# Optimization experiments

Hardware: AMD Instinct MI355X
Metric: run time of the kernel (lower is better)

The kernel has to match this reference:

```python
import jax, jax.numpy as jnp
import numpy as np

N_NODES = 100000
N_EDGES = 3200000
IN_CH = 256
OUT_CH = 10


def setup_inputs() -> dict:
    key = jax.random.key(0)
    k1, k2, k3, k4 = jax.random.split(key, 4)
    x = jax.random.normal(k1, (N_NODES, IN_CH), dtype=jnp.float32)
    edge_index = jax.random.randint(k2, (2, N_EDGES), 0, N_NODES, dtype=jnp.int64)
    W_mu = jax.random.normal(k3, (IN_CH, OUT_CH), dtype=jnp.float32) * (1.0 / np.sqrt(IN_CH))
    b_mu = jnp.zeros((OUT_CH,), dtype=jnp.float32)
    W_logstd = jax.random.normal(k4, (IN_CH, OUT_CH), dtype=jnp.float32) * (1.0 / np.sqrt(IN_CH))
    b_logstd = jnp.zeros((OUT_CH,), dtype=jnp.float32)
    return {"x": x, "edge_index": edge_index, "W_mu": W_mu, "b_mu": b_mu,
            "W_logstd": W_logstd, "b_logstd": b_logstd}


def _gcn_norm(edge_index, num_nodes):
    # PyG gcn_norm: add self loops, deg from target (col), norm = d^-1/2[row]*d^-1/2[col]
    loop = jnp.arange(num_nodes, dtype=edge_index.dtype)
    row = jnp.concatenate([edge_index[0], loop])  # source nodes
    col = jnp.concatenate([edge_index[1], loop])  # target nodes
    deg = jax.ops.segment_sum(jnp.ones_like(col, dtype=jnp.float32), col,
                              num_segments=num_nodes)
    dinv = jax.lax.rsqrt(jnp.maximum(deg, 1.0))  # self loops guarantee deg>=1
    norm = dinv[row] * dinv[col]  # [E+N]
    return row, col, norm


def _gcn_conv(x, W, b, row, col, norm, num_nodes):
    h = x @ W                               # [N, out]  linear transform first
    msg = h[row] * norm[:, None]            # gather + scale, [E+N, out]
    out = jax.ops.segment_sum(msg, col, num_segments=num_nodes)  # scatter-add
    return out + b


def reference(x, edge_index, W_mu, b_mu, W_logstd, b_logstd):
    n = x.shape[0]
    row, col, norm = _gcn_norm(edge_index, n)
    mu = _gcn_conv(x, W_mu, b_mu, row, col, norm, n)
    logstd = _gcn_conv(x, W_logstd, b_logstd, row, col, norm, n)
    return mu, logstd
```

## Files before the change

### kernel.cpp

```cpp
#include <hip/hip_runtime.h>
#include <math.h>

#define N_NODES 100000
#define N_EDGES 3200000
#define IN_CH 256
#define NC 20
#define OC 10
#define NPB 128
#define NBUCK 782
#define CAP 4864

#define CHUNK3 8192
#define NCHUNK3 391

__global__ __launch_bounds__(256) void k_initptr(int* __restrict__ bptr) {
    int i = blockIdx.x * 256 + threadIdx.x;
    if (i < NBUCK) bptr[i] = i * CAP;
}

__global__ __launch_bounds__(1024) void k_bin3(const int* __restrict__ row,
                                               const int* __restrict__ col,
                                               int* __restrict__ bptr,
                                               int* __restrict__ bpairs) {
    __shared__ int   lh[NBUCK];
    __shared__ int   lscan[NBUCK];
    __shared__ int   gmino[NBUCK];
    __shared__ int   stage[CHUNK3];
    __shared__ unsigned short sbkt[CHUNK3];

    int t = threadIdx.x;
    int e0 = blockIdx.x * CHUNK3;
    int nE = N_EDGES - e0; if (nE > CHUNK3) nE = CHUNK3;
    int n4 = nE >> 2;
    const int4* c4 = (const int4*)(col + e0);
    const int4* r4 = (const int4*)(row + e0);

    for (int i = t; i < NBUCK; i += 1024) lh[i] = 0;
    __syncthreads();

    for (int j = t; j < n4; j += 1024) {
        int4 c = c4[j];
        atomicAdd(&lh[c.x >> 7], 1); atomicAdd(&lh[c.y >> 7], 1);
        atomicAdd(&lh[c.z >> 7], 1); atomicAdd(&lh[c.w >> 7], 1);
    }
    __syncthreads();

    int cnt = 0;
    if (t < NBUCK) { cnt = lh[t]; lscan[t] = cnt; }
    __syncthreads();
    for (int o = 1; o < NBUCK; o <<= 1) {
        int add = 0;
        if (t < NBUCK && t >= o) add = lscan[t - o];
        __syncthreads();
        if (t < NBUCK) lscan[t] += add;
        __syncthreads();
    }
    if (t < NBUCK) {
        int lofs = lscan[t] - cnt;
        int gbase = cnt ? atomicAdd(&bptr[t], cnt) : 0;
        gmino[t] = gbase - lofs;
        lh[t] = lofs;
    }
    __syncthreads();

    for (int j = t; j < n4; j += 1024) {
        int4 c = c4[j];
        int4 r = r4[j];
        int b0 = c.x >> 7, b1 = c.y >> 7, b2 = c.z >> 7, b3 = c.w >> 7;
        int s0 = atomicAdd(&lh[b0], 1);
        int s1 = atomicAdd(&lh[b1], 1);
        int s2 = atomicAdd(&lh[b2], 1);
        int s3 = atomicAdd(&lh[b3], 1);
        stage[s0] = (r.x << 7) | (c.x & 127); sbkt[s0] = (unsigned short)b0;
        stage[s1] = (r.y << 7) | (c.y & 127); sbkt[s1] = (unsigned short)b1;
        stage[s2] = (r.z << 7) | (c.z & 127); sbkt[s2] = (unsigned short)b2;
        stage[s3] = (r.w << 7) | (c.w & 127); sbkt[s3] = (unsigned short)b3;
    }
    __syncthreads();

    for (int j = t; j < nE; j += 1024) {
        int b = sbkt[j];
        int dst = gmino[b] + j;
        if (dst < (b + 1) * CAP) bpairs[dst] = stage[j];
    }
}

__global__ __launch_bounds__(256) void k_deg(const int* __restrict__ bptr,
                                             const int* __restrict__ bpairs,
                                             float* __restrict__ dinv) {
    __shared__ int lc[NPB];
    int b = blockIdx.x, t = threadIdx.x;
    if (t < NPB) lc[t] = 0;
    __syncthreads();
    int start = b * CAP;
    int n = bptr[b] - start; if (n > CAP) n = CAP;
    for (int p = t; p < n; p += 256)
        atomicAdd(&lc[bpairs[start + p] & 127], 1);
    __syncthreads();
    int node = b * NPB + t;
    if (t < NPB && node < N_NODES)
        dinv[node] = rsqrtf((float)(lc[t] + 1));
}

__device__ __forceinline__ unsigned bfpack(float a, float b) {
    unsigned ua = __float_as_uint(a), ub = __float_as_uint(b);
    ua = (ua + 0x7FFFu + ((ua >> 16) & 1u)) >> 16;
    ub = (ub + 0x7FFFu + ((ub >> 16) & 1u)) >> 16;
    return ua | (ub << 16);
}
__device__ __forceinline__ float bflo(unsigned p) { return __uint_as_float(p << 16); }
__device__ __forceinline__ float bfhi(unsigned p) { return __uint_as_float(p & 0xFFFF0000u); }

__global__ __launch_bounds__(256) void k_gemm6s(const float* __restrict__ x,
                                                const float* __restrict__ Wmu,
                                                const float* __restrict__ Wls,
                                                const float* __restrict__ dinv,
                                                uint4* __restrict__ hbA,
                                                uint4* __restrict__ hbB,
                                                uint2* __restrict__ hbC) {
    __shared__ float sW[NC * 272];
    int t = threadIdx.x;
    for (int idx = t; idx < IN_CH * OC; idx += 256) {
        int k = idx / OC, c = idx - (idx / OC) * OC;
        int kk = k >> 6, j = k & 63;
        sW[c * 272 + kk * 68 + j]          = Wmu[idx];
        sW[(c + OC) * 272 + kk * 68 + j]   = Wls[idx];
    }
    __syncthreads();

    int kk = t & 3;
    int slot = t >> 2;
    int n0 = blockIdx.x * 128 + slot;

    int nd[2];
#pragma unroll
    for (int u = 0; u < 2; u++) {
        int n = n0 + u * 64;
        nd[u] = (n < N_NODES) ? n : (N_NODES - 1);
    }

    float acc[2][NC];
#pragma unroll
    for (int u = 0; u < 2; u++)
#pragma unroll
        for (int c = 0; c < NC; c++) acc[u][c] = 0.0f;

    const float4* x4 = (const float4*)x;

#pragma unroll 4
    for (int j4 = 0; j4 < 16; j4++) {
        float4 xv0 = x4[(size_t)nd[0] * 64 + kk * 16 + j4];
        float4 xv1 = x4[(size_t)nd[1] * 64 + kk * 16 + j4];
#pragma unroll
        for (int c = 0; c < NC; c++) {
            float4 w = *(const float4*)&sW[c * 272 + kk * 68 + j4 * 4];
            acc[0][c] += xv0.x * w.x + xv0.y * w.y + xv0.z * w.z + xv0.w * w.w;
            acc[1][c] += xv1.x * w.x + xv1.y * w.y + xv1.z * w.z + xv1.w * w.w;
        }
    }

#pragma unroll
    for (int u = 0; u < 2; u++)
#pragma unroll
        for (int c = 0; c < NC; c++) {
            acc[u][c] += __shfl_xor(acc[u][c], 2);
            acc[u][c] += __shfl_xor(acc[u][c], 1);
        }

    if (kk == 0) {
#pragma unroll
        for (int u = 0; u < 2; u++) {
            int n = n0 + u * 64;
            if (n >= N_NODES) continue;
            float d = dinv[n];
            hbA[n] = make_uint4(bfpack(acc[u][0] * d,  acc[u][1] * d),
                                bfpack(acc[u][2] * d,  acc[u][3] * d),
                                bfpack(acc[u][4] * d,  acc[u][5] * d),
                                bfpack(acc[u][6] * d,  acc[u][7] * d));
            hbB[n] = make_uint4(bfpack(acc[u][8] * d,  acc[u][9] * d),
                                bfpack(acc[u][10] * d, acc[u][11] * d),
                                bfpack(acc[u][12] * d, acc[u][13] * d),
                                bfpack(acc[u][14] * d, acc[u][15] * d));
            hbC[n] = make_uint2(bfpack(acc[u][16] * d, acc[u][17] * d),
                                bfpack(acc[u][18] * d, acc[u][19] * d));
        }
    }
}

__global__ __launch_bounds__(512) void k_agg7(const int* __restrict__ bptr,
                                              const int* __restrict__ bpairs,
                                              const uint4* __restrict__ hbA,
                                              const uint4* __restrict__ hbB,
                                              const uint2* __restrict__ hbC,
                                              const float* __restrict__ bmu,
                                              const float* __restrict__ bls,
                                              float* __restrict__ out) {
    __shared__ int lcnt[NPB];
    __shared__ int lscan[NPB];
    __shared__ int sCnt[NPB];
    __shared__ int ssrc[CAP];
    int b = blockIdx.x, t = threadIdx.x;
    int start = b * CAP;
    int n = bptr[b] - start; if (n > CAP) n = CAP;

    if (t < NPB) lcnt[t] = 0;
    __syncthreads();
    for (int p = t; p < n; p += 512)
        atomicAdd(&lcnt[bpairs[start + p] & 127], 1);
    __syncthreads();

    int cnt = 0;
    if (t < NPB) { cnt = lcnt[t]; lscan[t] = cnt; sCnt[t] = cnt; }
    __syncthreads();
    for (int o = 1; o < NPB; o <<= 1) {
        int add = 0;
        if (t < NPB && t >= o) add = lscan[t - o];
        __syncthreads();
        if (t < NPB) lscan[t] += add;
        __syncthreads();
    }
    if (t < NPB) lcnt[t] = lscan[t] - cnt;
    __syncthreads();

    for (int p = t; p < n; p += 512) {
        int pk = bpairs[start + p];
        int q = atomicAdd(&lcnt[pk & 127], 1);
        ssrc[q] = ((unsigned)pk) >> 7;
    }
    __syncthreads();

    int nl = t >> 2, quarter = t & 3;
    int node = b * NPB + nl;
    int ccnt = sCnt[nl];
    int base = lscan[nl] - ccnt;
    int j0 = (ccnt * quarter) >> 2;
    int j1 = (ccnt * (quarter + 1)) >> 2;

    float a[NC];
#pragma unroll
    for (int c = 0; c < NC; c++) a[c] = 0.0f;

#define ADDROW(R)                                                        \
    {                                                                    \
        uint4 qa = hbA[(R)];                                             \
        uint4 qb = hbB[(R)];                                             \
        uint2 qc = hbC[(R)];                                             \
        a[0]  += bflo(qa.x); a[1]  += bfhi(qa.x);                        \
        a[2]  += bflo(qa.y); a[3]  += bfhi(qa.y);                        \
        a[4]  += bflo(qa.z); a[5]  += bfhi(qa.z);                        \
        a[6]  += bflo(qa.w); a[7]  += bfhi(qa.w);                        \
        a[8]  += bflo(qb.x); a[9]  += bfhi(qb.x);                        \
        a[10] += bflo(qb.y); a[11] += bfhi(qb.y);                        \
        a[12] += bflo(qb.z); a[13] += bfhi(qb.z);                        \
        a[14] += bflo(qb.w); a[15] += bfhi(qb.w);                        \
        a[16] += bflo(qc.x); a[17] += bfhi(qc.x);                        \
        a[18] += bflo(qc.y); a[19] += bfhi(qc.y);                        \
    }

    int j = j0;
    for (; j + 1 < j1; j += 2) {
        int r0 = ssrc[base + j];
        int r1 = ssrc[base + j + 1];
        ADDROW(r0);
        ADDROW(r1);
    }
    if (j < j1) {
        int r0 = ssrc[base + j];
        ADDROW(r0);
    }
    if (quarter == 0 && node < N_NODES) ADDROW(node);
#undef ADDROW

#pragma unroll
    for (int c = 0; c < NC; c++) {
        a[c] += __shfl_xor(a[c], 1);
        a[c] += __shfl_xor(a[c], 2);
    }

    if (quarter == 0 && node < N_NODES) {
        float dn = rsqrtf((float)(ccnt + 1));
        float* om = out + (size_t)node * OC;
        float* ol = out + (size_t)N_NODES * OC + (size_t)node * OC;
#pragma unroll
        for (int c = 0; c < OC; c++) {
            om[c] = dn * a[c]      + bmu[c];
            ol[c] = dn * a[c + OC] + bls[c];
        }
    }
}

__global__ __launch_bounds__(256) void k_init_deg(float* __restrict__ deg) {
    int i = blockIdx.x * 256 + threadIdx.x;
    if (i < N_NODES) deg[i] = 1.0f;
}
__global__ __launch_bounds__(256) void k_count(const int* __restrict__ col, float* __restrict__ deg) {
    int e = blockIdx.x * 256 + threadIdx.x;
    if (e < N_EDGES) atomicAdd(&deg[col[e]], 1.0f);
}
__global__ __launch_bounds__(256) void k_dinvk(float* __restrict__ deg) {
    int i = blockIdx.x * 256 + threadIdx.x;
    if (i < N_NODES) deg[i] = rsqrtf(deg[i]);
}
__global__ __launch_bounds__(256) void k_gemm_f32(const float* __restrict__ x,
                                                  const float* __restrict__ Wmu,
                                                  const float* __restrict__ Wls,
                                                  float* __restrict__ h) {
    int node = blockIdx.x * 256 + threadIdx.x;
    if (node >= N_NODES) return;
    const float4* x4 = (const float4*)(x + (size_t)node * IN_CH);
    float acc[NC];
#pragma unroll
    for (int c = 0; c < NC; c++) acc[c] = 0.0f;
    for (int k4 = 0; k4 < IN_CH / 4; k4++) {
        float4 xv = x4[k4];
        float xk[4] = {xv.x, xv.y, xv.z, xv.w};
#pragma unroll
        for (int kk = 0; kk < 4; kk++) {
            const float* wm = Wmu + (k4 * 4 + kk) * OC;
            const float* wl = Wls + (k4 * 4 + kk) * OC;
#pragma unroll
            for (int c = 0; c < OC; c++) {
                acc[c]      += xk[kk] * wm[c];
                acc[c + OC] += xk[kk] * wl[c];
            }
        }
    }
    float* hp = h + (size_t)node * NC;
#pragma unroll
    for (int c = 0; c < NC; c++) hp[c] = acc[c];
}
__global__ __launch_bounds__(256) void k_scatter(const int* __restrict__ row, const int* __restrict__ col,
                                                 const float* __restrict__ dinv, const float* __restrict__ h,
                                                 float* __restrict__ out) {
    int e = blockIdx.x * 256 + threadIdx.x;
    if (e >= N_EDGES) return;
    int r = row[e], c = col[e];
    float s = dinv[r] * dinv[c];
    const float* hp = h + (size_t)r * NC;
    float* om = out + (size_t)c * OC;
    float* ol = om + (size_t)N_NODES * OC;
#pragma unroll
    for (int k = 0; k < OC; k++) atomicAdd(om + k, hp[k] * s);
#pragma unroll
    for (int k = 0; k < OC; k++) atomicAdd(ol + k, hp[OC + k] * s);
}
__global__ __launch_bounds__(256) void k_final(const float* __restrict__ h, const float* __restrict__ dinv,
                                               const float* __restrict__ bmu, const float* __restrict__ bls,
                                               float* __restrict__ out) {
    int i = blockIdx.x * 256 + threadIdx.x;
    if (i >= N_NODES * OC) return;
    int node = i / OC, c = i - node * OC;
    float d = dinv[node];
    float d2 = d * d;
    out[i]                += h[node * NC + c]      * d2 + bmu[c];
    out[N_NODES * OC + i] += h[node * NC + OC + c] * d2 + bls[c];
}

extern "C" void kernel_launch(void* const* d_in, const int* in_sizes, int n_in,
                              void* d_out, int out_size, void* d_ws, size_t ws_size,
                              hipStream_t stream) {
    const float* x   = (const float*)d_in[0];
    const int*   ei  = (const int*)d_in[1];
    const float* Wmu = (const float*)d_in[2];
    const float* bmu = (const float*)d_in[3];
    const float* Wls = (const float*)d_in[4];
    const float* bls = (const float*)d_in[5];
    float* out = (float*)d_out;

    const int* row = ei;
    const int* col = ei + N_EDGES;

    const size_t BPAIRS_OFF = (size_t)(9 << 19);
    const size_t REQ = BPAIRS_OFF + (size_t)NBUCK * CAP * 4;

    if (ws_size >= REQ) {
        char* w = (char*)d_ws;
        int*      bptr   = (int*)(w);
        float*    dinv   = (float*)(w + 8192);
        uint4*    hbA    = (uint4*)(w + (512 << 10));
        uint4*    hbB    = (uint4*)(w + (512 << 10) + 1600000);
        uint2*    hbC    = (uint2*)(w + (512 << 10) + 3200000);
        int*      bpairs = (int*)(w + BPAIRS_OFF);

        k_initptr<<<(NBUCK + 255) / 256, 256, 0, stream>>>(bptr);
        k_bin3<<<NCHUNK3, 1024, 0, stream>>>(row, col, bptr, bpairs);
        k_deg<<<NBUCK, 256, 0, stream>>>(bptr, bpairs, dinv);
        k_gemm6s<<<(N_NODES + 127) / 128, 256, 0, stream>>>(x, Wmu, Wls, dinv, hbA, hbB, hbC);
        k_agg7<<<NBUCK, 512, 0, stream>>>(bptr, bpairs, hbA, hbB, hbC, bmu, bls, out);
    } else {
        float* deg = (float*)d_ws;
        float* h   = (float*)((char*)d_ws + (1 << 20));
        hipMemsetAsync(d_out, 0, (size_t)out_size * sizeof(float), stream);
        k_init_deg<<<(N_NODES + 255) / 256, 256, 0, stream>>>(deg);
        k_count<<<(N_EDGES + 255) / 256, 256, 0, stream>>>(col, deg);
        k_dinvk<<<(N_NODES + 255) / 256, 256, 0, stream>>>(deg);
        k_gemm_f32<<<(N_NODES + 255) / 256, 256, 0, stream>>>(x, Wmu, Wls, h);
        k_scatter<<<(N_EDGES + 255) / 256, 256, 0, stream>>>(row, col, deg, h, out);
        k_final<<<(N_NODES * OC + 255) / 256, 256, 0, stream>>>(h, deg, bmu, bls, out);
    }
}
```

Baseline: 283.4 us.

## Fuse edge binning and GEMM into one heterogeneous kernel, move dinv scaling to aggregation

```diff
diff --git a/kernel.cpp b/kernel.cpp
--- a/kernel.cpp
+++ b/kernel.cpp
@@ -12,76 +12,170 @@
 
 #define CHUNK3 8192
 #define NCHUNK3 391
+#define NGEMMB 196
+#define NMEGA 587
 
 __global__ __launch_bounds__(256) void k_initptr(int* __restrict__ bptr) {
     int i = blockIdx.x * 256 + threadIdx.x;
     if (i < NBUCK) bptr[i] = i * CAP;
 }
 
-__global__ __launch_bounds__(1024) void k_bin3(const int* __restrict__ row,
+__device__ __forceinline__ unsigned bfpack(float a, float b) {
+    unsigned ua = __float_as_uint(a), ub = __float_as_uint(b);
+    ua = (ua + 0x7FFFu + ((ua >> 16) & 1u)) >> 16;
+    ub = (ub + 0x7FFFu + ((ub >> 16) & 1u)) >> 16;
+    return ua | (ub << 16);
+}
+__device__ __forceinline__ float bflo(unsigned p) { return __uint_as_float(p << 16); }
+__device__ __forceinline__ float bfhi(unsigned p) { return __uint_as_float(p & 0xFFFF0000u); }
+
+struct BinSmem {
+    int lh[NBUCK];
+    int lscan[NBUCK];
+    int gmino[NBUCK];
+    int stage[CHUNK3];
+    unsigned short sbkt[CHUNK3];
+};
+struct GemmSmem { float sW[NC * 272]; };
+union MegaSmem { BinSmem b; GemmSmem g; };
+
+__global__ __launch_bounds__(1024) void k_mega(const int* __restrict__ row,
                                                const int* __restrict__ col,
                                                int* __restrict__ bptr,
-                                               int* __restrict__ bpairs) {
-    __shared__ int   lh[NBUCK];
-    __shared__ int   lscan[NBUCK];
-    __shared__ int   gmino[NBUCK];
-    __shared__ int   stage[CHUNK3];
-    __shared__ unsigned short sbkt[CHUNK3];
-
+                                               int* __restrict__ bpairs,
+                                               const float* __restrict__ x,
+                                               const float* __restrict__ Wmu,
+                                               const float* __restrict__ Wls,
+                                               uint4* __restrict__ hbA,
+                                               uint4* __restrict__ hbB,
+                                               uint2* __restrict__ hbC) {
+    __shared__ MegaSmem sm;
+    int bid = blockIdx.x;
     int t = threadIdx.x;
-    int e0 = blockIdx.x * CHUNK3;
-    int nE = N_EDGES - e0; if (nE > CHUNK3) nE = CHUNK3;
-    int n4 = nE >> 2;
-    const int4* c4 = (const int4*)(col + e0);
-    const int4* r4 = (const int4*)(row + e0);
-
-    for (int i = t; i < NBUCK; i += 1024) lh[i] = 0;
-    __syncthreads();
-
-    for (int j = t; j < n4; j += 1024) {
-        int4 c = c4[j];
-        atomicAdd(&lh[c.x >> 7], 1); atomicAdd(&lh[c.y >> 7], 1);
-        atomicAdd(&lh[c.z >> 7], 1); atomicAdd(&lh[c.w >> 7], 1);
-    }
-    __syncthreads();
-
-    int cnt = 0;
-    if (t < NBUCK) { cnt = lh[t]; lscan[t] = cnt; }
-    __syncthreads();
-    for (int o = 1; o < NBUCK; o <<= 1) {
-        int add = 0;
-        if (t < NBUCK && t >= o) add = lscan[t - o];
-        __syncthreads();
-        if (t < NBUCK) lscan[t] += add;
-        __syncthreads();
-    }
-    if (t < NBUCK) {
-        int lofs = lscan[t] - cnt;
-        int gbase = cnt ? atomicAdd(&bptr[t], cnt) : 0;
-        gmino[t] = gbase - lofs;
-        lh[t] = lofs;
-    }
-    __syncthreads();
-
-    for (int j = t; j < n4; j += 1024) {
-        int4 c = c4[j];
-        int4 r = r4[j];
-        int b0 = c.x >> 7, b1 = c.y >> 7, b2 = c.z >> 7, b3 = c.w >> 7;
-        int s0 = atomicAdd(&lh[b0], 1);
-        int s1 = atomicAdd(&lh[b1], 1);
-        int s2 = atomicAdd(&lh[b2], 1);
-        int s3 = atomicAdd(&lh[b3], 1);
-        stage[s0] = (r.x << 7) | (c.x & 127); sbkt[s0] = (unsigned short)b0;
-        stage[s1] = (r.y << 7) | (c.y & 127); sbkt[s1] = (unsigned short)b1;
-        stage[s2] = (r.z << 7) | (c.z & 127); sbkt[s2] = (unsigned short)b2;
-        stage[s3] = (r.w << 7) | (c.w & 127); sbkt[s3] = (unsigned short)b3;
-    }
-    __syncthreads();
-
-    for (int j = t; j < nE; j += 1024) {
-        int b = sbkt[j];
-        int dst = gmino[b] + j;
-        if (dst < (b + 1) * CAP) bpairs[dst] = stage[j];
+    bool isGemm = (bid < 2 * NGEMMB) && (bid & 1);
+
+    if (!isGemm) {
+        int cb = (bid < 2 * NGEMMB) ? (bid >> 1) : (bid - NGEMMB);
+        int e0 = cb * CHUNK3;
+        int nE = N_EDGES - e0; if (nE > CHUNK3) nE = CHUNK3;
+        int n4 = nE >> 2;
+        const int4* c4 = (const int4*)(col + e0);
+        const int4* r4 = (const int4*)(row + e0);
+
+        for (int i = t; i < NBUCK; i += 1024) sm.b.lh[i] = 0;
+        __syncthreads();
+
+        for (int j = t; j < n4; j += 1024) {
+            int4 c = c4[j];
+            atomicAdd(&sm.b.lh[c.x >> 7], 1); atomicAdd(&sm.b.lh[c.y >> 7], 1);
+            atomicAdd(&sm.b.lh[c.z >> 7], 1); atomicAdd(&sm.b.lh[c.w >> 7], 1);
+        }
+        __syncthreads();
+
+        int cnt = 0;
+        if (t < NBUCK) { cnt = sm.b.lh[t]; sm.b.lscan[t] = cnt; }
+        __syncthreads();
+        for (int o = 1; o < NBUCK; o <<= 1) {
+            int add = 0;
+            if (t < NBUCK && t >= o) add = sm.b.lscan[t - o];
+            __syncthreads();
+            if (t < NBUCK) sm.b.lscan[t] += add;
+            __syncthreads();
+        }
+        if (t < NBUCK) {
+            int lofs = sm.b.lscan[t] - cnt;
+            int gbase = cnt ? atomicAdd(&bptr[t], cnt) : 0;
+            sm.b.gmino[t] = gbase - lofs;
+            sm.b.lh[t] = lofs;
+        }
+        __syncthreads();
+
+        for (int j = t; j < n4; j += 1024) {
+            int4 c = c4[j];
+            int4 r = r4[j];
+            int b0 = c.x >> 7, b1 = c.y >> 7, b2 = c.z >> 7, b3 = c.w >> 7;
+            int s0 = atomicAdd(&sm.b.lh[b0], 1);
+            int s1 = atomicAdd(&sm.b.lh[b1], 1);
+            int s2 = atomicAdd(&sm.b.lh[b2], 1);
+            int s3 = atomicAdd(&sm.b.lh[b3], 1);
+            sm.b.stage[s0] = (r.x << 7) | (c.x & 127); sm.b.sbkt[s0] = (unsigned short)b0;
+            sm.b.stage[s1] = (r.y << 7) | (c.y & 127); sm.b.sbkt[s1] = (unsigned short)b1;
+            sm.b.stage[s2] = (r.z << 7) | (c.z & 127); sm.b.sbkt[s2] = (unsigned short)b2;
+            sm.b.stage[s3] = (r.w << 7) | (c.w & 127); sm.b.sbkt[s3] = (unsigned short)b3;
+        }
+        __syncthreads();
+
+        for (int j = t; j < nE; j += 1024) {
+            int b = sm.b.sbkt[j];
+            int dst = sm.b.gmino[b] + j;
+            if (dst < (b + 1) * CAP) bpairs[dst] = sm.b.stage[j];
+        }
+    } else {
+        int gb = bid >> 1;
+        for (int idx = t; idx < IN_CH * OC; idx += 1024) {
+            int k = idx / OC, c = idx - (idx / OC) * OC;
+            int kk = k >> 6, j = k & 63;
+            sm.g.sW[c * 272 + kk * 68 + j]        = Wmu[idx];
+            sm.g.sW[(c + OC) * 272 + kk * 68 + j] = Wls[idx];
+        }
+        __syncthreads();
+
+        int kk = t & 3;
+        int slot = t >> 2;
+        int n0 = gb * 512 + slot;
+
+        int nd[2];
+#pragma unroll
+        for (int u = 0; u < 2; u++) {
+            int n = n0 + u * 256;
+            nd[u] = (n < N_NODES) ? n : (N_NODES - 1);
+        }
+
+        float acc[2][NC];
+#pragma unroll
+        for (int u = 0; u < 2; u++)
+#pragma unroll
+            for (int c = 0; c < NC; c++) acc[u][c] = 0.0f;
+
+        const float4* x4 = (const float4*)x;
+
+#pragma unroll 4
+        for (int j4 = 0; j4 < 16; j4++) {
+            float4 xv0 = x4[(size_t)nd[0] * 64 + kk * 16 + j4];
+            float4 xv1 = x4[(size_t)nd[1] * 64 + kk * 16 + j4];
+#pragma unroll
+            for (int c = 0; c < NC; c++) {
+                float4 w = *(const float4*)&sm.g.sW[c * 272 + kk * 68 + j4 * 4];
+                acc[0][c] += xv0.x * w.x + xv0.y * w.y + xv0.z * w.z + xv0.w * w.w;
+                acc[1][c] += xv1.x * w.x + xv1.y * w.y + xv1.z * w.z + xv1.w * w.w;
+            }
+        }
+
+#pragma unroll
+        for (int u = 0; u < 2; u++)
+#pragma unroll
+            for (int c = 0; c < NC; c++) {
+                acc[u][c] += __shfl_xor(acc[u][c], 2);
+                acc[u][c] += __shfl_xor(acc[u][c], 1);
+            }
+
+        if (kk == 0) {
+#pragma unroll
+            for (int u = 0; u < 2; u++) {
+                int n = n0 + u * 256;
+                if (n >= N_NODES) continue;
+                hbA[n] = make_uint4(bfpack(acc[u][0],  acc[u][1]),
+                                    bfpack(acc[u][2],  acc[u][3]),
+                                    bfpack(acc[u][4],  acc[u][5]),
+                                    bfpack(acc[u][6],  acc[u][7]));
+                hbB[n] = make_uint4(bfpack(acc[u][8],  acc[u][9]),
+                                    bfpack(acc[u][10], acc[u][11]),
+                                    bfpack(acc[u][12], acc[u][13]),
+                                    bfpack(acc[u][14], acc[u][15]));
+                hbC[n] = make_uint2(bfpack(acc[u][16], acc[u][17]),
+                                    bfpack(acc[u][18], acc[u][19]));
+            }
+        }
     }
 }
 
@@ -102,96 +196,12 @@
         dinv[node] = rsqrtf((float)(lc[t] + 1));
 }
 
-__device__ __forceinline__ unsigned bfpack(float a, float b) {
-    unsigned ua = __float_as_uint(a), ub = __float_as_uint(b);
-    ua = (ua + 0x7FFFu + ((ua >> 16) & 1u)) >> 16;
-    ub = (ub + 0x7FFFu + ((ub >> 16) & 1u)) >> 16;
-    return ua | (ub << 16);
-}
-__device__ __forceinline__ float bflo(unsigned p) { return __uint_as_float(p << 16); }
-__device__ __forceinline__ float bfhi(unsigned p) { return __uint_as_float(p & 0xFFFF0000u); }
-
-__global__ __launch_bounds__(256) void k_gemm6s(const float* __restrict__ x,
-                                                const float* __restrict__ Wmu,
-                                                const float* __restrict__ Wls,
-                                                const float* __restrict__ dinv,
-                                                uint4* __restrict__ hbA,
-                                                uint4* __restrict__ hbB,
-                                                uint2* __restrict__ hbC) {
-    __shared__ float sW[NC * 272];
-    int t = threadIdx.x;
-    for (int idx = t; idx < IN_CH * OC; idx += 256) {
-        int k = idx / OC, c = idx - (idx / OC) * OC;
-        int kk = k >> 6, j = k & 63;
-        sW[c * 272 + kk * 68 + j]          = Wmu[idx];
-        sW[(c + OC) * 272 + kk * 68 + j]   = Wls[idx];
-    }
-    __syncthreads();
-
-    int kk = t & 3;
-    int slot = t >> 2;
-    int n0 = blockIdx.x * 128 + slot;
-
-    int nd[2];
-#pragma unroll
-    for (int u = 0; u < 2; u++) {
-        int n = n0 + u * 64;
-        nd[u] = (n < N_NODES) ? n : (N_NODES - 1);
-    }
-
-    float acc[2][NC];
-#pragma unroll
-    for (int u = 0; u < 2; u++)
-#pragma unroll
-        for (int c = 0; c < NC; c++) acc[u][c] = 0.0f;
-
-    const float4* x4 = (const float4*)x;
-
-#pragma unroll 4
-    for (int j4 = 0; j4 < 16; j4++) {
-        float4 xv0 = x4[(size_t)nd[0] * 64 + kk * 16 + j4];
-        float4 xv1 = x4[(size_t)nd[1] * 64 + kk * 16 + j4];
-#pragma unroll
-        for (int c = 0; c < NC; c++) {
-            float4 w = *(const float4*)&sW[c * 272 + kk * 68 + j4 * 4];
-            acc[0][c] += xv0.x * w.x + xv0.y * w.y + xv0.z * w.z + xv0.w * w.w;
-            acc[1][c] += xv1.x * w.x + xv1.y * w.y + xv1.z * w.z + xv1.w * w.w;
-        }
-    }
-
-#pragma unroll
-    for (int u = 0; u < 2; u++)
-#pragma unroll
-        for (int c = 0; c < NC; c++) {
-            acc[u][c] += __shfl_xor(acc[u][c], 2);
-            acc[u][c] += __shfl_xor(acc[u][c], 1);
-        }
-
-    if (kk == 0) {
-#pragma unroll
-        for (int u = 0; u < 2; u++) {
-            int n = n0 + u * 64;
-            if (n >= N_NODES) continue;
-            float d = dinv[n];
-            hbA[n] = make_uint4(bfpack(acc[u][0] * d,  acc[u][1] * d),
-                                bfpack(acc[u][2] * d,  acc[u][3] * d),
-                                bfpack(acc[u][4] * d,  acc[u][5] * d),
-                                bfpack(acc[u][6] * d,  acc[u][7] * d));
-            hbB[n] = make_uint4(bfpack(acc[u][8] * d,  acc[u][9] * d),
-                                bfpack(acc[u][10] * d, acc[u][11] * d),
-                                bfpack(acc[u][12] * d, acc[u][13] * d),
-                                bfpack(acc[u][14] * d, acc[u][15] * d));
-            hbC[n] = make_uint2(bfpack(acc[u][16] * d, acc[u][17] * d),
-                                bfpack(acc[u][18] * d, acc[u][19] * d));
-        }
-    }
-}
-
-__global__ __launch_bounds__(512) void k_agg7(const int* __restrict__ bptr,
+__global__ __launch_bounds__(512) void k_agg8(const int* __restrict__ bptr,
                                               const int* __restrict__ bpairs,
                                               const uint4* __restrict__ hbA,
                                               const uint4* __restrict__ hbB,
                                               const uint2* __restrict__ hbC,
+                                              const float* __restrict__ dinv,
                                               const float* __restrict__ bmu,
                                               const float* __restrict__ bls,
                                               float* __restrict__ out) {
@@ -240,35 +250,38 @@
 #pragma unroll
     for (int c = 0; c < NC; c++) a[c] = 0.0f;
 
-#define ADDROW(R)                                                        \
+#define ADDROW(R, S)                                                     \
     {                                                                    \
         uint4 qa = hbA[(R)];                                             \
         uint4 qb = hbB[(R)];                                             \
         uint2 qc = hbC[(R)];                                             \
-        a[0]  += bflo(qa.x); a[1]  += bfhi(qa.x);                        \
-        a[2]  += bflo(qa.y); a[3]  += bfhi(qa.y);                        \
-        a[4]  += bflo(qa.z); a[5]  += bfhi(qa.z);                        \
-        a[6]  += bflo(qa.w); a[7]  += bfhi(qa.w);                        \
-        a[8]  += bflo(qb.x); a[9]  += bfhi(qb.x);                        \
-        a[10] += bflo(qb.y); a[11] += bfhi(qb.y);                        \
-        a[12] += bflo(qb.z); a[13] += bfhi(qb.z);                        \
-        a[14] += bflo(qb.w); a[15] += bfhi(qb.w);                        \
-        a[16] += bflo(qc.x); a[17] += bfhi(qc.x);                        \
-        a[18] += bflo(qc.y); a[19] += bfhi(qc.y);                        \
+        float s_ = (S);                                                  \
+        a[0]  += s_ * bflo(qa.x); a[1]  += s_ * bfhi(qa.x);              \
+        a[2]  += s_ * bflo(qa.y); a[3]  += s_ * bfhi(qa.y);              \
+        a[4]  += s_ * bflo(qa.z); a[5]  += s_ * bfhi(qa.z);              \
+        a[6]  += s_ * bflo(qa.w); a[7]  += s_ * bfhi(qa.w);              \
+        a[8]  += s_ * bflo(qb.x); a[9]  += s_ * bfhi(qb.x);              \
+        a[10] += s_ * bflo(qb.y); a[11] += s_ * bfhi(qb.y);              \
+        a[12] += s_ * bflo(qb.z); a[13] += s_ * bfhi(qb.z);              \
+        a[14] += s_ * bflo(qb.w); a[15] += s_ * bfhi(qb.w);              \
+        a[16] += s_ * bflo(qc.x); a[17] += s_ * bfhi(qc.x);              \
+        a[18] += s_ * bflo(qc.y); a[19] += s_ * bfhi(qc.y);              \
     }
 
     int j = j0;
     for (; j + 1 < j1; j += 2) {
         int r0 = ssrc[base + j];
         int r1 = ssrc[base + j + 1];
-        ADDROW(r0);
-        ADDROW(r1);
+        float s0 = dinv[r0];
+        float s1 = dinv[r1];
+        ADDROW(r0, s0);
+        ADDROW(r1, s1);
     }
     if (j < j1) {
         int r0 = ssrc[base + j];
-        ADDROW(r0);
-    }
-    if (quarter == 0 && node < N_NODES) ADDROW(node);
+        ADDROW(r0, dinv[r0]);
+    }
+    if (quarter == 0 && node < N_NODES) ADDROW(node, dinv[node]);
 #undef ADDROW
 
 #pragma unroll
@@ -383,10 +396,9 @@
         int*      bpairs = (int*)(w + BPAIRS_OFF);
 
         k_initptr<<<(NBUCK + 255) / 256, 256, 0, stream>>>(bptr);
-        k_bin3<<<NCHUNK3, 1024, 0, stream>>>(row, col, bptr, bpairs);
+        k_mega<<<NMEGA, 1024, 0, stream>>>(row, col, bptr, bpairs, x, Wmu, Wls, hbA, hbB, hbC);
         k_deg<<<NBUCK, 256, 0, stream>>>(bptr, bpairs, dinv);
-        k_gemm6s<<<(N_NODES + 127) / 128, 256, 0, stream>>>(x, Wmu, Wls, dinv, hbA, hbB, hbC);
-        k_agg7<<<NBUCK, 512, 0, stream>>>(bptr, bpairs, hbA, hbB, hbC, bmu, bls, out);
+        k_agg8<<<NBUCK, 512, 0, stream>>>(bptr, bpairs, hbA, hbB, hbC, dinv, bmu, bls, out);
     } else {
         float* deg = (float*)d_ws;
         float* h   = (float*)((char*)d_ws + (1 << 20));
```

Result: slower. 309.9 us (+9.3%).

## Fuse edge binning and GEMM into one interleaved launch, defer dinv scaling

Applied to the files above, without the earlier changes.

```diff
diff --git a/kernel.cpp b/kernel.cpp
--- a/kernel.cpp
+++ b/kernel.cpp
@@ -12,94 +12,12 @@
 
 #define CHUNK3 8192
 #define NCHUNK3 391
+#define NGEMMB 196
+#define NMEGA 587
 
 __global__ __launch_bounds__(256) void k_initptr(int* __restrict__ bptr) {
     int i = blockIdx.x * 256 + threadIdx.x;
     if (i < NBUCK) bptr[i] = i * CAP;
-}
-
-__global__ __launch_bounds__(1024) void k_bin3(const int* __restrict__ row,
-                                               const int* __restrict__ col,
-                                               int* __restrict__ bptr,
-                                               int* __restrict__ bpairs) {
-    __shared__ int   lh[NBUCK];
-    __shared__ int   lscan[NBUCK];
-    __shared__ int   gmino[NBUCK];
-    __shared__ int   stage[CHUNK3];
-    __shared__ unsigned short sbkt[CHUNK3];
-
-    int t = threadIdx.x;
-    int e0 = blockIdx.x * CHUNK3;
-    int nE = N_EDGES - e0; if (nE > CHUNK3) nE = CHUNK3;
-    int n4 = nE >> 2;
-    const int4* c4 = (const int4*)(col + e0);
-    const int4* r4 = (const int4*)(row + e0);
-
-    for (int i = t; i < NBUCK; i += 1024) lh[i] = 0;
-    __syncthreads();
-
-    for (int j = t; j < n4; j += 1024) {
-        int4 c = c4[j];
-        atomicAdd(&lh[c.x >> 7], 1); atomicAdd(&lh[c.y >> 7], 1);
-        atomicAdd(&lh[c.z >> 7], 1); atomicAdd(&lh[c.w >> 7], 1);
-    }
-    __syncthreads();
-
-    int cnt = 0;
-    if (t < NBUCK) { cnt = lh[t]; lscan[t] = cnt; }
-    __syncthreads();
-    for (int o = 1; o < NBUCK; o <<= 1) {
-        int add = 0;
-        if (t < NBUCK && t >= o) add = lscan[t - o];
-        __syncthreads();
-        if (t < NBUCK) lscan[t] += add;
-        __syncthreads();
-    }
-    if (t < NBUCK) {
-        int lofs = lscan[t] - cnt;
-        int gbase = cnt ? atomicAdd(&bptr[t], cnt) : 0;
-        gmino[t] = gbase - lofs;
-        lh[t] = lofs;
-    }
-    __syncthreads();
-
-    for (int j = t; j < n4; j += 1024) {
-        int4 c = c4[j];
-        int4 r = r4[j];
-        int b0 = c.x >> 7, b1 = c.y >> 7, b2 = c.z >> 7, b3 = c.w >> 7;
-        int s0 = atomicAdd(&lh[b0], 1);
-        int s1 = atomicAdd(&lh[b1], 1);
-        int s2 = atomicAdd(&lh[b2], 1);
-        int s3 = atomicAdd(&lh[b3], 1);
-        stage[s0] = (r.x << 7) | (c.x & 127); sbkt[s0] = (unsigned short)b0;
-        stage[s1] = (r.y << 7) | (c.y & 127); sbkt[s1] = (unsigned short)b1;
-        stage[s2] = (r.z << 7) | (c.z & 127); sbkt[s2] = (unsigned short)b2;
-        stage[s3] = (r.w << 7) | (c.w & 127); sbkt[s3] = (unsigned short)b3;
-    }
-    __syncthreads();
-
-    for (int j = t; j < nE; j += 1024) {
-        int b = sbkt[j];
-        int dst = gmino[b] + j;
-        if (dst < (b + 1) * CAP) bpairs[dst] = stage[j];
-    }
-}
-
-__global__ __launch_bounds__(256) void k_deg(const int* __restrict__ bptr,
-                                             const int* __restrict__ bpairs,
-                                             float* __restrict__ dinv) {
-    __shared__ int lc[NPB];
-    int b = blockIdx.x, t = threadIdx.x;
-    if (t < NPB) lc[t] = 0;
-    __syncthreads();
-    int start = b * CAP;
-    int n = bptr[b] - start; if (n > CAP) n = CAP;
-    for (int p = t; p < n; p += 256)
-        atomicAdd(&lc[bpairs[start + p] & 127], 1);
-    __syncthreads();
-    int node = b * NPB + t;
-    if (t < NPB && node < N_NODES)
-        dinv[node] = rsqrtf((float)(lc[t] + 1));
 }
 
 __device__ __forceinline__ unsigned bfpack(float a, float b) {
@@ -111,79 +29,179 @@
 __device__ __forceinline__ float bflo(unsigned p) { return __uint_as_float(p << 16); }
 __device__ __forceinline__ float bfhi(unsigned p) { return __uint_as_float(p & 0xFFFF0000u); }
 
-__global__ __launch_bounds__(256) void k_gemm6s(const float* __restrict__ x,
-                                                const float* __restrict__ Wmu,
-                                                const float* __restrict__ Wls,
-                                                const float* __restrict__ dinv,
-                                                uint4* __restrict__ hbA,
-                                                uint4* __restrict__ hbB,
-                                                uint2* __restrict__ hbC) {
-    __shared__ float sW[NC * 272];
+struct BinSmem {
+    int lh[NBUCK];
+    int lscan[NBUCK];
+    int gmino[NBUCK];
+    int stage[CHUNK3];
+    unsigned short sbkt[CHUNK3];
+};
+struct GemmSmem { float sW[NC * 272]; };
+union MegaSmem { BinSmem b; GemmSmem g; };
+
+__global__ __launch_bounds__(1024) void k_mega32(const int* __restrict__ row,
+                                                 const int* __restrict__ col,
+                                                 int* __restrict__ bptr,
+                                                 int* __restrict__ bpairs,
+                                                 const float* __restrict__ x,
+                                                 const float* __restrict__ Wmu,
+                                                 const float* __restrict__ Wls,
+                                                 float* __restrict__ h32) {
+    __shared__ MegaSmem sm;
+    int bid = blockIdx.x;
     int t = threadIdx.x;
-    for (int idx = t; idx < IN_CH * OC; idx += 256) {
-        int k = idx / OC, c = idx - (idx / OC) * OC;
-        int kk = k >> 6, j = k & 63;
-        sW[c * 272 + kk * 68 + j]          = Wmu[idx];
-        sW[(c + OC) * 272 + kk * 68 + j]   = Wls[idx];
-    }
-    __syncthreads();
-
-    int kk = t & 3;
-    int slot = t >> 2;
-    int n0 = blockIdx.x * 128 + slot;
-
-    int nd[2];
-#pragma unroll
-    for (int u = 0; u < 2; u++) {
-        int n = n0 + u * 64;
-        nd[u] = (n < N_NODES) ? n : (N_NODES - 1);
-    }
-
-    float acc[2][NC];
-#pragma unroll
-    for (int u = 0; u < 2; u++)
-#pragma unroll
-        for (int c = 0; c < NC; c++) acc[u][c] = 0.0f;
-
-    const float4* x4 = (const float4*)x;
+    bool isGemm = (bid < 2 * NGEMMB) && (bid & 1);
+
+    if (!isGemm) {
+        int cb = (bid < 2 * NGEMMB) ? (bid >> 1) : (bid - NGEMMB);
+        int e0 = cb * CHUNK3;
+        int nE = N_EDGES - e0; if (nE > CHUNK3) nE = CHUNK3;
+        int n4 = nE >> 2;
+        const int4* c4 = (const int4*)(col + e0);
+        const int4* r4 = (const int4*)(row + e0);
+
+        for (int i = t; i < NBUCK; i += 1024) sm.b.lh[i] = 0;
+        __syncthreads();
+
+        for (int j = t; j < n4; j += 1024) {
+            int4 c = c4[j];
+            atomicAdd(&sm.b.lh[c.x >> 7], 1); atomicAdd(&sm.b.lh[c.y >> 7], 1);
+            atomicAdd(&sm.b.lh[c.z >> 7], 1); atomicAdd(&sm.b.lh[c.w >> 7], 1);
+        }
+        __syncthreads();
+
+        int cnt = 0;
+        if (t < NBUCK) { cnt = sm.b.lh[t]; sm.b.lscan[t] = cnt; }
+        __syncthreads();
+        for (int o = 1; o < NBUCK; o <<= 1) {
+            int add = 0;
+            if (t < NBUCK && t >= o) add = sm.b.lscan[t - o];
+            __syncthreads();
+            if (t < NBUCK) sm.b.lscan[t] += add;
+            __syncthreads();
+        }
+        if (t < NBUCK) {
+            int lofs = sm.b.lscan[t] - cnt;
+            int gbase = cnt ? atomicAdd(&bptr[t], cnt) : 0;
+            sm.b.gmino[t] = gbase - lofs;
+            sm.b.lh[t] = lofs;
+        }
+        __syncthreads();
+
+        for (int j = t; j < n4; j += 1024) {
+            int4 c = c4[j];
+            int4 r = r4[j];
+            int b0 = c.x >> 7, b1 = c.y >> 7, b2 = c.z >> 7, b3 = c.w >> 7;
+            int s0 = atomicAdd(&sm.b.lh[b0], 1);
+            int s1 = atomicAdd(&sm.b.lh[b1], 1);
+            int s2 = atomicAdd(&sm.b.lh[b2], 1);
+            int s3 = atomicAdd(&sm.b.lh[b3], 1);
+            sm.b.stage[s0] = (r.x << 7) | (c.x & 127); sm.b.sbkt[s0] = (unsigned short)b0;
+            sm.b.stage[s1] = (r.y << 7) | (c.y & 127); sm.b.sbkt[s1] = (unsigned short)b1;
+            sm.b.stage[s2] = (r.z << 7) | (c.z & 127); sm.b.sbkt[s2] = (unsigned short)b2;
+            sm.b.stage[s3] = (r.w << 7) | (c.w & 127); sm.b.sbkt[s3] = (unsigned short)b3;
+        }
+        __syncthreads();
+
+        for (int j = t; j < nE; j += 1024) {
+            int b = sm.b.sbkt[j];
+            int dst = sm.b.gmino[b] + j;
+            if (dst < (b + 1) * CAP) bpairs[dst] = sm.b.stage[j];
+        }
+    } else {
+        int gb = bid >> 1;
+        for (int idx = t; idx < IN_CH * OC; idx += 1024) {
+            int k = idx / OC, c = idx - (idx / OC) * OC;
+            int kk = k >> 6, j = k & 63;
+            sm.g.sW[c * 272 + kk * 68 + j]        = Wmu[idx];
+            sm.g.sW[(c + OC) * 272 + kk * 68 + j] = Wls[idx];
+        }
+        __syncthreads();
+
+        int kk = t & 3;
+        int slot = t >> 2;
+        int n0 = gb * 512 + slot;
+
+        int nd[2];
+#pragma unroll
+        for (int u = 0; u < 2; u++) {
+            int n = n0 + u * 256;
+            nd[u] = (n < N_NODES) ? n : (N_NODES - 1);
+        }
+
+        float acc[2][NC];
+#pragma unroll
+        for (int u = 0; u < 2; u++)
+#pragma unroll
+            for (int c = 0; c < NC; c++) acc[u][c] = 0.0f;
+
+        const float4* x4 = (const float4*)x;
 
 #pragma unroll 4
-    for (int j4 = 0; j4 < 16; j4++) {
-        float4 xv0 = x4[(size_t)nd[0] * 64 + kk * 16 + j4];
-        float4 xv1 = x4[(size_t)nd[1] * 64 + kk * 16 + j4];
-#pragma unroll
-        for (int c = 0; c < NC; c++) {
-            float4 w = *(const float4*)&sW[c * 272 + kk * 68 + j4 * 4];
-            acc[0][c] += xv0.x * w.x + xv0.y * w.y + xv0.z * w.z + xv0.w * w.w;
-            acc[1][c] += xv1.x * w.x + xv1.y * w.y + xv1.z * w.z + xv1.w * w.w;
-        }
-    }
-
-#pragma unroll
-    for (int u = 0; u < 2; u++)
-#pragma unroll
-        for (int c = 0; c < NC; c++) {
-            acc[u][c] += __shfl_xor(acc[u][c], 2);
-            acc[u][c] += __shfl_xor(acc[u][c], 1);
-        }
-
-    if (kk == 0) {
-#pragma unroll
-        for (int u = 0; u < 2; u++) {
-            int n = n0 + u * 64;
-            if (n >= N_NODES) continue;
-            float d = dinv[n];
-            hbA[n] = make_uint4(bfpack(acc[u][0] * d,  acc[u][1] * d),
-                                bfpack(acc[u][2] * d,  acc[u][3] * d),
-                                bfpack(acc[u][4] * d,  acc[u][5] * d),
-                                bfpack(acc[u][6] * d,  acc[u][7] * d));
-            hbB[n] = make_uint4(bfpack(acc[u][8] * d,  acc[u][9] * d),
-                                bfpack(acc[u][10] * d, acc[u][11] * d),
-                                bfpack(acc[u][12] * d, acc[u][13] * d),
-                                bfpack(acc[u][14] * d, acc[u][15] * d));
-            hbC[n] = make_uint2(bfpack(acc[u][16] * d, acc[u][17] * d),
-                                bfpack(acc[u][18] * d, acc[u][19] * d));
-        }
+        for (int j4 = 0; j4 < 16; j4++) {
+            float4 xv0 = x4[(size_t)nd[0] * 64 + kk * 16 + j4];
+            float4 xv1 = x4[(size_t)nd[1] * 64 + kk * 16 + j4];
+#pragma unroll
+            for (int c = 0; c < NC; c++) {
+                float4 w = *(const float4*)&sm.g.sW[c * 272 + kk * 68 + j4 * 4];
+                acc[0][c] += xv0.x * w.x + xv0.y * w.y + xv0.z * w.z + xv0.w * w.w;
+                acc[1][c] += xv1.x * w.x + xv1.y * w.y + xv1.z * w.z + xv1.w * w.w;
+            }
+        }
+
+#pragma unroll
+        for (int u = 0; u < 2; u++)
+#pragma unroll
+            for (int c = 0; c < NC; c++) {
+                acc[u][c] += __shfl_xor(acc[u][c], 2);
+                acc[u][c] += __shfl_xor(acc[u][c], 1);
+            }
+
+        if (kk == 0) {
+#pragma unroll
+            for (int u = 0; u < 2; u++) {
+                int n = n0 + u * 256;
+                if (n >= N_NODES) continue;
+                float* hp = h32 + (size_t)n * NC;
+                *(float4*)(hp + 0)  = make_float4(acc[u][0],  acc[u][1],  acc[u][2],  acc[u][3]);
+                *(float4*)(hp + 4)  = make_float4(acc[u][4],  acc[u][5],  acc[u][6],  acc[u][7]);
+                *(float4*)(hp + 8)  = make_float4(acc[u][8],  acc[u][9],  acc[u][10], acc[u][11]);
+                *(float4*)(hp + 12) = make_float4(acc[u][12], acc[u][13], acc[u][14], acc[u][15]);
+                *(float4*)(hp + 16) = make_float4(acc[u][16], acc[u][17], acc[u][18], acc[u][19]);
+            }
+        }
+    }
+}
+
+__global__ __launch_bounds__(256) void k_degs(const int* __restrict__ bptr,
+                                              const int* __restrict__ bpairs,
+                                              const float* __restrict__ h32,
+                                              uint4* __restrict__ hbA,
+                                              uint4* __restrict__ hbB,
+                                              uint2* __restrict__ hbC) {
+    __shared__ int lc[NPB];
+    int b = blockIdx.x, t = threadIdx.x;
+    if (t < NPB) lc[t] = 0;
+    __syncthreads();
+    int start = b * CAP;
+    int n = bptr[b] - start; if (n > CAP) n = CAP;
+    for (int p = t; p < n; p += 256)
+        atomicAdd(&lc[bpairs[start + p] & 127], 1);
+    __syncthreads();
+    int node = b * NPB + t;
+    if (t < NPB && node < N_NODES) {
+        float d = rsqrtf((float)(lc[t] + 1));
+        const float* hp = h32 + (size_t)node * NC;
+        float4 v0 = *(const float4*)(hp + 0);
+        float4 v1 = *(const float4*)(hp + 4);
+        float4 v2 = *(const float4*)(hp + 8);
+        float4 v3 = *(const float4*)(hp + 12);
+        float4 v4 = *(const float4*)(hp + 16);
+        hbA[node] = make_uint4(bfpack(v0.x * d, v0.y * d), bfpack(v0.z * d, v0.w * d),
+                               bfpack(v1.x * d, v1.y * d), bfpack(v1.z * d, v1.w * d));
+        hbB[node] = make_uint4(bfpack(v2.x * d, v2.y * d), bfpack(v2.z * d, v2.w * d),
+                               bfpack(v3.x * d, v3.y * d), bfpack(v3.z * d, v3.w * d));
+        hbC[node] = make_uint2(bfpack(v4.x * d, v4.y * d), bfpack(v4.z * d, v4.w * d));
     }
 }
 
@@ -289,6 +307,162 @@
     }
 }
 
+__global__ __launch_bounds__(1024) void k_bin3(const int* __restrict__ row,
+                                               const int* __restrict__ col,
+                                               int* __restrict__ bptr,
+                                               int* __restrict__ bpairs) {
+    __shared__ int   lh[NBUCK];
+    __shared__ int   lscan[NBUCK];
+    __shared__ int   gmino[NBUCK];
+    __shared__ int   stage[CHUNK3];
+    __shared__ unsigned short sbkt[CHUNK3];
+
+    int t = threadIdx.x;
+    int e0 = blockIdx.x * CHUNK3;
+    int nE = N_EDGES - e0; if (nE > CHUNK3) nE = CHUNK3;
+    int n4 = nE >> 2;
+    const int4* c4 = (const int4*)(col + e0);
+    const int4* r4 = (const int4*)(row + e0);
+
+    for (int i = t; i < NBUCK; i += 1024) lh[i] = 0;
+    __syncthreads();
+    for (int j = t; j < n4; j += 1024) {
+        int4 c = c4[j];
+        atomicAdd(&lh[c.x >> 7], 1); atomicAdd(&lh[c.y >> 7], 1);
+        atomicAdd(&lh[c.z >> 7], 1); atomicAdd(&lh[c.w >> 7], 1);
+    }
+    __syncthreads();
+    int cnt = 0;
+    if (t < NBUCK) { cnt = lh[t]; lscan[t] = cnt; }
+    __syncthreads();
+    for (int o = 1; o < NBUCK; o <<= 1) {
+        int add = 0;
+        if (t < NBUCK && t >= o) add = lscan[t - o];
+        __syncthreads();
+        if (t < NBUCK) lscan[t] += add;
+        __syncthreads();
+    }
+    if (t < NBUCK) {
+        int lofs = lscan[t] - cnt;
+        int gbase = cnt ? atomicAdd(&bptr[t], cnt) : 0;
+        gmino[t] = gbase - lofs;
+        lh[t] = lofs;
+    }
+    __syncthreads();
+    for (int j = t; j < n4; j += 1024) {
+        int4 c = c4[j];
+        int4 r = r4[j];
+        int b0 = c.x >> 7, b1 = c.y >> 7, b2 = c.z >> 7, b3 = c.w >> 7;
+        int s0 = atomicAdd(&lh[b0], 1);
+        int s1 = atomicAdd(&lh[b1], 1);
+        int s2 = atomicAdd(&lh[b2], 1);
+        int s3 = atomicAdd(&lh[b3], 1);
+        stage[s0] = (r.x << 7) | (c.x & 127); sbkt[s0] = (unsigned short)b0;
+        stage[s1] = (r.y << 7) | (c.y & 127); sbkt[s1] = (unsigned short)b1;
+        stage[s2] = (r.z << 7) | (c.z & 127); sbkt[s2] = (unsigned short)b2;
+        stage[s3] = (r.w << 7) | (c.w & 127); sbkt[s3] = (unsigned short)b3;
+    }
+    __syncthreads();
+    for (int j = t; j < nE; j += 1024) {
+        int b = sbkt[j];
+        int dst = gmino[b] + j;
+        if (dst < (b + 1) * CAP) bpairs[dst] = stage[j];
+    }
+}
+
+__global__ __launch_bounds__(256) void k_deg(const int* __restrict__ bptr,
+                                             const int* __restrict__ bpairs,
+                                             float* __restrict__ dinv) {
+    __shared__ int lc[NPB];
+    int b = blockIdx.x, t = threadIdx.x;
+    if (t < NPB) lc[t] = 0;
+    __syncthreads();
+    int start = b * CAP;
+    int n = bptr[b] - start; if (n > CAP) n = CAP;
+    for (int p = t; p < n; p += 256)
+        atomicAdd(&lc[bpairs[start + p] & 127], 1);
+    __syncthreads();
+    int node = b * NPB + t;
+    if (t < NPB && node < N_NODES)
+        dinv[node] = rsqrtf((float)(lc[t] + 1));
+}
+
+__global__ __launch_bounds__(256) void k_gemm6s(const float* __restrict__ x,
+                                                const float* __restrict__ Wmu,
+                                                const float* __restrict__ Wls,
+                                                const float* __restrict__ dinv,
+                                                uint4* __restrict__ hbA,
+                                                uint4* __restrict__ hbB,
+                                                uint2* __restrict__ hbC) {
+    __shared__ float sW[NC * 272];
+    int t = threadIdx.x;
+    for (int idx = t; idx < IN_CH * OC; idx += 256) {
+        int k = idx / OC, c = idx - (idx / OC) * OC;
+        int kk = k >> 6, j = k & 63;
+        sW[c * 272 + kk * 68 + j]          = Wmu[idx];
+        sW[(c + OC) * 272 + kk * 68 + j]   = Wls[idx];
+    }
+    __syncthreads();
+
+    int kk = t & 3;
+    int slot = t >> 2;
+    int n0 = blockIdx.x * 128 + slot;
+
+    int nd[2];
+#pragma unroll
+    for (int u = 0; u < 2; u++) {
+        int n = n0 + u * 64;
+        nd[u] = (n < N_NODES) ? n : (N_NODES - 1);
+    }
+
+    float acc[2][NC];
+#pragma unroll
+    for (int u = 0; u < 2; u++)
+#pragma unroll
+        for (int c = 0; c < NC; c++) acc[u][c] = 0.0f;
+
+    const float4* x4 = (const float4*)x;
+
+#pragma unroll 4
+    for (int j4 = 0; j4 < 16; j4++) {
+        float4 xv0 = x4[(size_t)nd[0] * 64 + kk * 16 + j4];
+        float4 xv1 = x4[(size_t)nd[1] * 64 + kk * 16 + j4];
+#pragma unroll
+        for (int c = 0; c < NC; c++) {
+            float4 w = *(const float4*)&sW[c * 272 + kk * 68 + j4 * 4];
+            acc[0][c] += xv0.x * w.x + xv0.y * w.y + xv0.z * w.z + xv0.w * w.w;
+            acc[1][c] += xv1.x * w.x + xv1.y * w.y + xv1.z * w.z + xv1.w * w.w;
+        }
+    }
+
+#pragma unroll
+    for (int u = 0; u < 2; u++)
+#pragma unroll
+        for (int c = 0; c < NC; c++) {
+            acc[u][c] += __shfl_xor(acc[u][c], 2);
+            acc[u][c] += __shfl_xor(acc[u][c], 1);
+        }
+
+    if (kk == 0) {
+#pragma unroll
+        for (int u = 0; u < 2; u++) {
+            int n = n0 + u * 64;
+            if (n >= N_NODES) continue;
+            float d = dinv[n];
+            hbA[n] = make_uint4(bfpack(acc[u][0] * d,  acc[u][1] * d),
+                                bfpack(acc[u][2] * d,  acc[u][3] * d),
+                                bfpack(acc[u][4] * d,  acc[u][5] * d),
+                                bfpack(acc[u][6] * d,  acc[u][7] * d));
+            hbB[n] = make_uint4(bfpack(acc[u][8] * d,  acc[u][9] * d),
+                                bfpack(acc[u][10] * d, acc[u][11] * d),
+                                bfpack(acc[u][12] * d, acc[u][13] * d),
+                                bfpack(acc[u][14] * d, acc[u][15] * d));
+            hbC[n] = make_uint2(bfpack(acc[u][16] * d, acc[u][17] * d),
+                                bfpack(acc[u][18] * d, acc[u][19] * d));
+        }
+    }
+}
+
 __global__ __launch_bounds__(256) void k_init_deg(float* __restrict__ deg) {
     int i = blockIdx.x * 256 + threadIdx.x;
     if (i < N_NODES) deg[i] = 1.0f;
@@ -371,9 +545,24 @@
     const int* col = ei + N_EDGES;
 
     const size_t BPAIRS_OFF = (size_t)(9 << 19);
-    const size_t REQ = BPAIRS_OFF + (size_t)NBUCK * CAP * 4;
-
-    if (ws_size >= REQ) {
+    const size_t REQ  = BPAIRS_OFF + (size_t)NBUCK * CAP * 4;
+    const size_t H32_OFF = (size_t)20 << 20;
+    const size_t REQ2 = H32_OFF + (size_t)N_NODES * NC * 4;
+
+    if (ws_size >= REQ2) {
+        char* w = (char*)d_ws;
+        int*      bptr   = (int*)(w);
+        uint4*    hbA    = (uint4*)(w + (512 << 10));
+        uint4*    hbB    = (uint4*)(w + (512 << 10) + 1600000);
+        uint2*    hbC    = (uint2*)(w + (512 << 10) + 3200000);
+        int*      bpairs = (int*)(w + BPAIRS_OFF);
+        float*    h32    = (float*)(w + H32_OFF);
+
+        k_initptr<<<(NBUCK + 255) / 256, 256, 0, stream>>>(bptr);
+        k_mega32<<<NMEGA, 1024, 0, stream>>>(row, col, bptr, bpairs, x, Wmu, Wls, h32);
+        k_degs<<<NBUCK, 256, 0, stream>>>(bptr, bpairs, h32, hbA, hbB, hbC);
+        k_agg7<<<NBUCK, 512, 0, stream>>>(bptr, bpairs, hbA, hbB, hbC, bmu, bls, out);
+    } else if (ws_size >= REQ) {
         char* w = (char*)d_ws;
         int*      bptr   = (int*)(w);
         float*    dinv   = (float*)(w + 8192);
```

New measurement: 297.4 us. 4.9% more time.
